# Kernel tuning notes

Hardware: AMD Instinct MI355X
Metric: run time of the kernel (lower is better)

## Reference

```python
import jax, jax.numpy as jnp
import numpy as np

B, C, H, W = 8, 8, 512, 512


def setup_inputs() -> dict:
    key = jax.random.key(0)
    k1, k2 = jax.random.split(key)
    logits = jax.random.normal(k1, (B, C, H, W), dtype=jnp.float32)
    target = jax.random.normal(k2, (B, C, H, W), dtype=jnp.float32)
    return {"logits": logits, "target": target}


def _hausdorff_one(x, y):
    # x, y: [H, W] -> H points in R^W (rows are points), euclidean metric,
    # matching hausdorff.hausdorff_distance on a 2D array.
    x2 = jnp.sum(x * x, axis=-1)  # [H]
    y2 = jnp.sum(y * y, axis=-1)  # [H]
    # squared pairwise distances via GEMM identity; clamp negatives from fp error
    d2 = jnp.maximum(x2[:, None] + y2[None, :] - 2.0 * (x @ y.T), 0.0)  # [H, H]
    d = jnp.sqrt(d2)
    fwd = jnp.max(jnp.min(d, axis=1))  # sup_x inf_y
    bwd = jnp.max(jnp.min(d, axis=0))  # sup_y inf_x
    return jnp.maximum(fwd, bwd)


def reference(logits, target):
    lx = jnp.argmax(logits, axis=1).astype(jnp.float32)  # [B, H, W] label maps
    ty = jnp.argmax(target, axis=1).astype(jnp.float32)  # [B, H, W]
    hd = jax.vmap(_hausdorff_one)(lx, ty)  # [B]
    return jnp.mean(hd)
```

## Files before the change

### kernel.cpp

```cpp
#include <hip/hip_runtime.h>
#include <hip/hip_bf16.h>
#include <climits>

#define HWSZ 262144
#define CHWSZ 2097152

typedef short short8 __attribute__((ext_vector_type(8)));
typedef float f32x4 __attribute__((ext_vector_type(4)));

__global__ __launch_bounds__(256) void hd_init(float* x2, float* y2, int* rowmin, int* colmin) {
    int i = blockIdx.x * 256 + threadIdx.x;
    x2[i] = 0.0f;
    y2[i] = 0.0f;
    rowmin[i] = INT_MAX;
    colmin[i] = INT_MAX;
}

__global__ __launch_bounds__(256) void hd_argmax(const float* __restrict__ logits,
                                                 const float* __restrict__ target,
                                                 ushort* __restrict__ lxb,
                                                 ushort* __restrict__ tyb,
                                                 float* __restrict__ x2,
                                                 float* __restrict__ y2) {
    int t = blockIdx.x * 256 + threadIdx.x;
    int p = t << 2;
    int b = p >> 18;
    int off = p & (HWSZ - 1);
    int h = off >> 9;
    int lane = threadIdx.x & 63;

    {
        const float4* L = (const float4*)(logits + (size_t)b * CHWSZ + off);
        float4 bv = L[0];
        int ix = 0, iy = 0, iz = 0, iw = 0;
#pragma unroll
        for (int c = 1; c < 8; ++c) {
            float4 v = L[c * (HWSZ / 4)];
            if (v.x > bv.x) { bv.x = v.x; ix = c; }
            if (v.y > bv.y) { bv.y = v.y; iy = c; }
            if (v.z > bv.z) { bv.z = v.z; iz = c; }
            if (v.w > bv.w) { bv.w = v.w; iw = c; }
        }
        ushort4 ub;
        ub.x = (ushort)(__float_as_uint((float)ix) >> 16);
        ub.y = (ushort)(__float_as_uint((float)iy) >> 16);
        ub.z = (ushort)(__float_as_uint((float)iz) >> 16);
        ub.w = (ushort)(__float_as_uint((float)iw) >> 16);
        *(ushort4*)(lxb + p) = ub;
        int s = ix*ix + iy*iy + iz*iz + iw*iw;
#pragma unroll
        for (int o = 32; o > 0; o >>= 1) s += __shfl_down(s, o, 64);
        if (lane == 0) atomicAdd(&x2[(b << 9) + h], (float)s);
    }
    {
        const float4* T = (const float4*)(target + (size_t)b * CHWSZ + off);
        float4 bv = T[0];
        int ix = 0, iy = 0, iz = 0, iw = 0;
#pragma unroll
        for (int c = 1; c < 8; ++c) {
            float4 v = T[c * (HWSZ / 4)];
            if (v.x > bv.x) { bv.x = v.x; ix = c; }
            if (v.y > bv.y) { bv.y = v.y; iy = c; }
            if (v.z > bv.z) { bv.z = v.z; iz = c; }
            if (v.w > bv.w) { bv.w = v.w; iw = c; }
        }
        ushort4 ub;
        ub.x = (ushort)(__float_as_uint((float)ix) >> 16);
        ub.y = (ushort)(__float_as_uint((float)iy) >> 16);
        ub.z = (ushort)(__float_as_uint((float)iz) >> 16);
        ub.w = (ushort)(__float_as_uint((float)iw) >> 16);
        *(ushort4*)(tyb + p) = ub;
        int s = ix*ix + iy*iy + iz*iz + iw*iw;
#pragma unroll
        for (int o = 32; o > 0; o >>= 1) s += __shfl_down(s, o, 64);
        if (lane == 0) atomicAdd(&y2[(b << 9) + h], (float)s);
    }
}

__global__ __launch_bounds__(256) void hd_dist(const ushort* __restrict__ lxb,
                                               const ushort* __restrict__ tyb,
                                               const float* __restrict__ x2,
                                               const float* __restrict__ y2,
                                               int* __restrict__ rowmin,
                                               int* __restrict__ colmin) {
    int b = blockIdx.y;
    int ti = blockIdx.x >> 3, tj = blockIdx.x & 7;
    int tid = threadIdx.x;
    int l = tid & 63;
    int wv = tid >> 6;
    int wr = wv >> 1, wc = wv & 1;
    int lr = l & 15, lg = l >> 4;

    const ushort* X = lxb + b * HWSZ + (ti * 64 + wr * 32 + lr) * 512 + lg * 8;
    const ushort* Y = tyb + b * HWSZ + (tj * 64 + wc * 32 + lr) * 512 + lg * 8;

    f32x4 acc00 = {0.f, 0.f, 0.f, 0.f};
    f32x4 acc01 = {0.f, 0.f, 0.f, 0.f};
    f32x4 acc10 = {0.f, 0.f, 0.f, 0.f};
    f32x4 acc11 = {0.f, 0.f, 0.f, 0.f};

#pragma unroll 4
    for (int kk = 0; kk < 512; kk += 32) {
        short8 a0 = *(const short8*)(X + kk);
        short8 a1 = *(const short8*)(X + 8192 + kk);
        short8 b0 = *(const short8*)(Y + kk);
        short8 b1 = *(const short8*)(Y + 8192 + kk);
        acc00 = __builtin_amdgcn_mfma_f32_16x16x32_bf16(a0, b0, acc00, 0, 0, 0);
        acc01 = __builtin_amdgcn_mfma_f32_16x16x32_bf16(a0, b1, acc01, 0, 0, 0);
        acc10 = __builtin_amdgcn_mfma_f32_16x16x32_bf16(a1, b0, acc10, 0, 0, 0);
        acc11 = __builtin_amdgcn_mfma_f32_16x16x32_bf16(a1, b1, acc11, 0, 0, 0);
    }

    int rb = (b << 9) + ti * 64 + wr * 32;
    int cb = (b << 9) + tj * 64 + wc * 32;
    float x2v0[4], x2v1[4];
#pragma unroll
    for (int r = 0; r < 4; ++r) {
        x2v0[r] = x2[rb + lg * 4 + r];
        x2v1[r] = x2[rb + 16 + lg * 4 + r];
    }
    float y2v0 = y2[cb + lr];
    float y2v1 = y2[cb + 16 + lr];

    int d2[2][2][4];
#pragma unroll
    for (int r = 0; r < 4; ++r) {
        d2[0][0][r] = (int)(fmaxf(fmaf(-2.0f, acc00[r], x2v0[r] + y2v0), 0.0f) + 0.5f);
        d2[0][1][r] = (int)(fmaxf(fmaf(-2.0f, acc01[r], x2v0[r] + y2v1), 0.0f) + 0.5f);
        d2[1][0][r] = (int)(fmaxf(fmaf(-2.0f, acc10[r], x2v1[r] + y2v0), 0.0f) + 0.5f);
        d2[1][1][r] = (int)(fmaxf(fmaf(-2.0f, acc11[r], x2v1[r] + y2v1), 0.0f) + 0.5f);
    }

#pragma unroll
    for (int fi = 0; fi < 2; ++fi) {
#pragma unroll
        for (int r = 0; r < 4; ++r) {
            int m = min(d2[fi][0][r], d2[fi][1][r]);
            m = min(m, __shfl_xor(m, 1, 64));
            m = min(m, __shfl_xor(m, 2, 64));
            m = min(m, __shfl_xor(m, 4, 64));
            m = min(m, __shfl_xor(m, 8, 64));
            if (lr == 0) atomicMin(&rowmin[rb + fi * 16 + lg * 4 + r], m);
        }
    }
#pragma unroll
    for (int fj = 0; fj < 2; ++fj) {
        int m;
        if (fj == 0) {
            m = min(min(min(d2[0][0][0], d2[0][0][1]), min(d2[0][0][2], d2[0][0][3])),
                    min(min(d2[1][0][0], d2[1][0][1]), min(d2[1][0][2], d2[1][0][3])));
        } else {
            m = min(min(min(d2[0][1][0], d2[0][1][1]), min(d2[0][1][2], d2[0][1][3])),
                    min(min(d2[1][1][0], d2[1][1][1]), min(d2[1][1][2], d2[1][1][3])));
        }
        m = min(m, __shfl_xor(m, 16, 64));
        m = min(m, __shfl_xor(m, 32, 64));
        if (lg == 0) atomicMin(&colmin[cb + fj * 16 + lr], m);
    }
}

__global__ __launch_bounds__(512) void hd_final(const int* __restrict__ rowmin,
                                                const int* __restrict__ colmin,
                                                float* __restrict__ out) {
    int w = threadIdx.x >> 6, l = threadIdx.x & 63;
    int m = 0;
#pragma unroll
    for (int j = 0; j < 512; j += 64) {
        m = max(m, rowmin[(w << 9) + j + l]);
        m = max(m, colmin[(w << 9) + j + l]);
    }
#pragma unroll
    for (int s = 32; s > 0; s >>= 1) m = max(m, __shfl_xor(m, s, 64));
    __shared__ float hd[8];
    if (l == 0) hd[w] = sqrtf((float)m);
    __syncthreads();
    if (threadIdx.x == 0) {
        float s = 0.0f;
#pragma unroll
        for (int i = 0; i < 8; ++i) s += hd[i];
        out[0] = s * 0.125f;
    }
}

extern "C" void kernel_launch(void* const* d_in, const int* in_sizes, int n_in,
                              void* d_out, int out_size, void* d_ws, size_t ws_size,
                              hipStream_t stream) {
    (void)in_sizes; (void)n_in; (void)out_size; (void)ws_size;
    const float* logits = (const float*)d_in[0];
    const float* target = (const float*)d_in[1];

    char* ws = (char*)d_ws;
    ushort* lxb = (ushort*)ws;
    ushort* tyb = (ushort*)(ws + (4u << 20));
    float* x2   = (float*)(ws + (8u << 20));
    float* y2   = x2 + 4096;
    int* rowmin = (int*)(y2 + 4096);
    int* colmin = rowmin + 4096;
    float* out  = (float*)d_out;

    hipLaunchKernelGGL(hd_init,   dim3(16),    dim3(256), 0, stream, x2, y2, rowmin, colmin);
    hipLaunchKernelGGL(hd_argmax, dim3(2048),  dim3(256), 0, stream, logits, target, lxb, tyb, x2, y2);
    hipLaunchKernelGGL(hd_dist,   dim3(64, 8), dim3(256), 0, stream, lxb, tyb, x2, y2, rowmin, colmin);
    hipLaunchKernelGGL(hd_final,  dim3(1),     dim3(512), 0, stream, rowmin, colmin, out);
}
```

Baseline: 51.52 us.

## Split row-norm computation into separate kernel and widen argmax loads

```diff
diff --git a/kernel.cpp b/kernel.cpp
--- a/kernel.cpp
+++ b/kernel.cpp
@@ -7,11 +7,11 @@
 
 typedef short short8 __attribute__((ext_vector_type(8)));
 typedef float f32x4 __attribute__((ext_vector_type(4)));
-
-__global__ __launch_bounds__(256) void hd_init(float* x2, float* y2, int* rowmin, int* colmin) {
+typedef float f4 __attribute__((ext_vector_type(4)));
+typedef unsigned short u16x8 __attribute__((ext_vector_type(8)));
+
+__global__ __launch_bounds__(256) void hd_init(int* rowmin, int* colmin) {
     int i = blockIdx.x * 256 + threadIdx.x;
-    x2[i] = 0.0f;
-    y2[i] = 0.0f;
     rowmin[i] = INT_MAX;
     colmin[i] = INT_MAX;
 }
@@ -19,61 +19,84 @@
 __global__ __launch_bounds__(256) void hd_argmax(const float* __restrict__ logits,
                                                  const float* __restrict__ target,
                                                  ushort* __restrict__ lxb,
-                                                 ushort* __restrict__ tyb,
-                                                 float* __restrict__ x2,
-                                                 float* __restrict__ y2) {
+                                                 ushort* __restrict__ tyb) {
     int t = blockIdx.x * 256 + threadIdx.x;
-    int p = t << 2;
+    int p = t << 3;
     int b = p >> 18;
     int off = p & (HWSZ - 1);
-    int h = off >> 9;
-    int lane = threadIdx.x & 63;
-
-    {
-        const float4* L = (const float4*)(logits + (size_t)b * CHWSZ + off);
-        float4 bv = L[0];
-        int ix = 0, iy = 0, iz = 0, iw = 0;
-#pragma unroll
-        for (int c = 1; c < 8; ++c) {
-            float4 v = L[c * (HWSZ / 4)];
-            if (v.x > bv.x) { bv.x = v.x; ix = c; }
-            if (v.y > bv.y) { bv.y = v.y; iy = c; }
-            if (v.z > bv.z) { bv.z = v.z; iz = c; }
-            if (v.w > bv.w) { bv.w = v.w; iw = c; }
-        }
-        ushort4 ub;
-        ub.x = (ushort)(__float_as_uint((float)ix) >> 16);
-        ub.y = (ushort)(__float_as_uint((float)iy) >> 16);
-        ub.z = (ushort)(__float_as_uint((float)iz) >> 16);
-        ub.w = (ushort)(__float_as_uint((float)iw) >> 16);
-        *(ushort4*)(lxb + p) = ub;
-        int s = ix*ix + iy*iy + iz*iz + iw*iw;
-#pragma unroll
-        for (int o = 32; o > 0; o >>= 1) s += __shfl_down(s, o, 64);
-        if (lane == 0) atomicAdd(&x2[(b << 9) + h], (float)s);
-    }
-    {
-        const float4* T = (const float4*)(target + (size_t)b * CHWSZ + off);
-        float4 bv = T[0];
-        int ix = 0, iy = 0, iz = 0, iw = 0;
-#pragma unroll
-        for (int c = 1; c < 8; ++c) {
-            float4 v = T[c * (HWSZ / 4)];
-            if (v.x > bv.x) { bv.x = v.x; ix = c; }
-            if (v.y > bv.y) { bv.y = v.y; iy = c; }
-            if (v.z > bv.z) { bv.z = v.z; iz = c; }
-            if (v.w > bv.w) { bv.w = v.w; iw = c; }
-        }
-        ushort4 ub;
-        ub.x = (ushort)(__float_as_uint((float)ix) >> 16);
-        ub.y = (ushort)(__float_as_uint((float)iy) >> 16);
-        ub.z = (ushort)(__float_as_uint((float)iz) >> 16);
-        ub.w = (ushort)(__float_as_uint((float)iw) >> 16);
-        *(ushort4*)(tyb + p) = ub;
-        int s = ix*ix + iy*iy + iz*iz + iw*iw;
-#pragma unroll
-        for (int o = 32; o > 0; o >>= 1) s += __shfl_down(s, o, 64);
-        if (lane == 0) atomicAdd(&y2[(b << 9) + h], (float)s);
+
+    const f4* L = (const f4*)(logits + (size_t)b * CHWSZ + off);
+    const f4* T = (const f4*)(target + (size_t)b * CHWSZ + off);
+
+    f4 v[16];
+#pragma unroll
+    for (int c = 0; c < 8; ++c) {
+        v[2 * c]     = L[c * (HWSZ / 4)];
+        v[2 * c + 1] = L[c * (HWSZ / 4) + 1];
+    }
+    u16x8 ub;
+#pragma unroll
+    for (int half = 0; half < 2; ++half) {
+#pragma unroll
+        for (int j = 0; j < 4; ++j) {
+            float bv = v[half][j];
+            int bi = 0;
+#pragma unroll
+            for (int c = 1; c < 8; ++c) {
+                float x = v[2 * c + half][j];
+                bool g = x > bv;
+                bv = g ? x : bv;
+                bi = g ? c : bi;
+            }
+            ub[half * 4 + j] = (ushort)(__float_as_uint((float)bi) >> 16);
+        }
+    }
+    *(u16x8*)(lxb + p) = ub;
+
+    f4 w[16];
+#pragma unroll
+    for (int c = 0; c < 8; ++c) {
+        w[2 * c]     = T[c * (HWSZ / 4)];
+        w[2 * c + 1] = T[c * (HWSZ / 4) + 1];
+    }
+    u16x8 wb;
+#pragma unroll
+    for (int half = 0; half < 2; ++half) {
+#pragma unroll
+        for (int j = 0; j < 4; ++j) {
+            float bv = w[half][j];
+            int bi = 0;
+#pragma unroll
+            for (int c = 1; c < 8; ++c) {
+                float x = w[2 * c + half][j];
+                bool g = x > bv;
+                bv = g ? x : bv;
+                bi = g ? c : bi;
+            }
+            wb[half * 4 + j] = (ushort)(__float_as_uint((float)bi) >> 16);
+        }
+    }
+    *(u16x8*)(tyb + p) = wb;
+}
+
+__global__ __launch_bounds__(256) void hd_norms(const ushort* __restrict__ lxb,
+                                                const ushort* __restrict__ tyb,
+                                                float* __restrict__ x2,
+                                                float* __restrict__ y2) {
+    int wid = blockIdx.x * 4 + (threadIdx.x >> 6);
+    int l = threadIdx.x & 63;
+    const ushort* src = (wid < 4096) ? (lxb + wid * 512) : (tyb + (wid - 4096) * 512);
+    u16x8 u = *(const u16x8*)(src + l * 8);
+    float s = 0.0f;
+#pragma unroll
+    for (int j = 0; j < 8; ++j) {
+        float f = __uint_as_float((unsigned)u[j] << 16);
+        s += f * f;
+    }
+#pragma unroll
+    for (int o = 32; o > 0; o >>= 1) s += __shfl_xor(s, o, 64);
+    if (l == 0) {
+        if (wid < 4096) x2[wid] = s; else y2[wid - 4096] = s;
     }
 }
 
@@ -198,8 +221,9 @@
     int* colmin = rowmin + 4096;
     float* out  = (float*)d_out;
 
-    hipLaunchKernelGGL(hd_init,   dim3(16),    dim3(256), 0, stream, x2, y2, rowmin, colmin);
-    hipLaunchKernelGGL(hd_argmax, dim3(2048),  dim3(256), 0, stream, logits, target, lxb, tyb, x2, y2);
+    hipLaunchKernelGGL(hd_init,   dim3(16),    dim3(256), 0, stream, rowmin, colmin);
+    hipLaunchKernelGGL(hd_argmax, dim3(1024),  dim3(256), 0, stream, logits, target, lxb, tyb);
+    hipLaunchKernelGGL(hd_norms,  dim3(2048),  dim3(256), 0, stream, lxb, tyb, x2, y2);
     hipLaunchKernelGGL(hd_dist,   dim3(64, 8), dim3(256), 0, stream, lxb, tyb, x2, y2, rowmin, colmin);
     hipLaunchKernelGGL(hd_final,  dim3(1),     dim3(512), 0, stream, rowmin, colmin, out);
 }
```

Result: slower. 59.03 us (+14.6%).
